# Kernel optimization log

Hardware: AMD Instinct MI355X
Metric: run time of the kernel (lower is better)

## Reference

```python
import jax, jax.numpy as jnp
import numpy as np

# TT configuration (matches init_kwargs)
P = (100, 100, 100)      # tt_p_shapes, prod = num_embeddings = 1e6
Q = (4, 4, 8)            # tt_q_shapes, prod = embedding_dim = 128
R = (1, 32, 32, 1)       # tt_ranks padded with boundary 1s
D = 128                  # embedding_dim
B = 4096                 # batch size (number of bags)
H = 50                   # pooling factor (history length)
NNZ = B * H              # total indices


def setup_inputs() -> dict:
    key = jax.random.key(0)
    k1, k2, k3, k4 = jax.random.split(key, 4)
    # TT cores, stored flattened along trailing dims like TT-Rec:
    # core_i : [p_i, r_i * q_i * r_{i+1}]
    sigma = 0.1
    core0 = sigma * jax.random.normal(k1, (P[0], R[0] * Q[0] * R[1]), dtype=jnp.float32)
    core1 = sigma * jax.random.normal(k2, (P[1], R[1] * Q[1] * R[2]), dtype=jnp.float32)
    core2 = sigma * jax.random.normal(k3, (P[2], R[2] * Q[2] * R[3]), dtype=jnp.float32)
    indices = jax.random.randint(k4, (NNZ,), 0, P[0] * P[1] * P[2], dtype=jnp.int32)
    lengths = jnp.full((B,), H, dtype=jnp.int32)
    return {"indices": indices, "lengths": lengths,
            "core0": core0, "core1": core1, "core2": core2}


def reference(indices, lengths, core0, core1, core2):
    n = indices.shape[0]
    # mixed-radix decomposition of flat row index over p-shapes
    i1 = indices // (P[1] * P[2])
    i2 = (indices // P[2]) % P[1]
    i3 = indices % P[2]
    # gather per-index TT core slices
    a = core0[i1].reshape(n, Q[0], R[1])          # [n, q1, r1]
    b = core1[i2].reshape(n, R[1], Q[1], R[2])    # [n, r1, q2, r2]
    c = core2[i3].reshape(n, R[2], Q[2])          # [n, r2, q3]
    # TT contraction chain reconstructing each embedding row
    ab = jnp.einsum('nar,nrbs->nabs', a, b).reshape(n, Q[0] * Q[1], R[2])  # [n, q1*q2, r2]
    emb = jnp.einsum('nms,nsc->nmc', ab, c).reshape(n, D)                  # [n, D]
    # bag sum-pooling: rowidx = repeat_interleave(arange(B), lengths)
    batch = lengths.shape[0]
    rowidx = jnp.repeat(jnp.arange(batch, dtype=jnp.int32), lengths,
                        total_repeat_length=n)
    out = jax.ops.segment_sum(emb, rowidx, num_segments=batch)             # [B, D]
    return out
```

## Files before the change

### kernel.cpp

```cpp
#include <hip/hip_runtime.h>
#include <hip/hip_bf16.h>


#define P0 100
#define P1 100
#define P2 100
#define Q0 4
#define Q1 4
#define Q2 8
#define DIM 128
#define NPAIR (P0 * P1)

typedef __attribute__((ext_vector_type(8))) short short8v;
typedef __attribute__((ext_vector_type(4))) float f32x4;

__global__ __launch_bounds__(128) void prep(const int* __restrict__ lengths, int B,
                                            const float* __restrict__ core0,
                                            const float* __restrict__ core1,
                                            const float* __restrict__ core2,
                                            int* __restrict__ offsets,
                                            __hip_bfloat16* __restrict__ bfrag,
                                            __hip_bfloat16* __restrict__ ab) {
    int bid = blockIdx.x;
    int t = threadIdx.x;
    if (bid == 0) {
        __shared__ int part[128];
        int per = (B + 127) / 128;
        int s = 0;
        for (int k = 0; k < per; ++k) {
            int i = t * per + k;
            s += (i < B) ? lengths[i] : 0;
        }
        part[t] = s;
        __syncthreads();
        for (int d = 1; d < 128; d <<= 1) {
            int v = (t >= d) ? part[t - d] : 0;
            __syncthreads();
            part[t] += v;
            __syncthreads();
        }
        int run = part[t] - s;
        for (int k = 0; k < per; ++k) {
            int i = t * per + k;
            if (i < B) { offsets[i] = run; run += lengths[i]; }
        }
        if (t == 127) offsets[B] = part[127];
    } else if (bid <= P2) {
        if (t < 64 && !(t & 8)) {
            int i3 = bid - 1;
            int h = t >> 4, c3 = t & 7;
            const float* crow = core2 + (size_t)i3 * (32 * Q2);
            __hip_bfloat16* o = bfrag + (size_t)i3 * 256 + h * 64 + c3 * 8;
#pragma unroll
            for (int j = 0; j < 8; ++j)
                o[j] = __float2bfloat16(crow[(h * 8 + j) * Q2 + c3]);
        }
    } else {
        int p12 = bid - 1 - P2;
        int i1 = p12 / P1;
        int i2 = p12 - i1 * P1;
        __shared__ float a_lds[128];
        a_lds[t] = core0[i1 * 128 + t];
        __syncthreads();
        const float* brow = core1 + (size_t)i2 * 4096;
        float acc0 = 0.f, acc1 = 0.f, acc2 = 0.f, acc3 = 0.f;
#pragma unroll
        for (int r = 0; r < 32; ++r) {
            float bv = brow[r * 128 + t];
            acc0 += a_lds[r] * bv;
            acc1 += a_lds[32 + r] * bv;
            acc2 += a_lds[64 + r] * bv;
            acc3 += a_lds[96 + r] * bv;
        }
        __hip_bfloat16* o = ab + (size_t)p12 * 512;
        o[t]       = __float2bfloat16(acc0);
        o[128 + t] = __float2bfloat16(acc1);
        o[256 + t] = __float2bfloat16(acc2);
        o[384 + t] = __float2bfloat16(acc3);
    }
}

__global__ __launch_bounds__(256, 6) void bag_pool(const int* __restrict__ indices, int n,
                                                   const int* __restrict__ offsets, int B,
                                                   const char* __restrict__ ab,
                                                   const char* __restrict__ bfrag,
                                                   float* __restrict__ out) {
    int w = threadIdx.x >> 6;
    int lane = threadIdx.x & 63;
    int bag = blockIdx.x * 2 + (w >> 1);
    int half = w & 1;

    int start = 0, end = 0;
    if (bag < B) {
        start = offsets[bag];
        end = offsets[bag + 1];
        if (bag == B - 1 && end < n) end = n;
        if (end > n) end = n;
        if (start > n) start = n;
        if (end < start) end = start;
    }
    int cnt = end - start;
    int c0 = (cnt + 1) >> 1;
    int mystart = start + (half ? c0 : 0);
    int mycnt = half ? (cnt - c0) : c0;

    int aoff = (lane & 15) * 64 + (lane >> 4) * 16;
    int boff = (lane >> 4) * 128 + (lane & 7) * 16;

    f32x4 acc0 = {0.f, 0.f, 0.f, 0.f};
    f32x4 acc1 = {0.f, 0.f, 0.f, 0.f};
    f32x4 acc2 = {0.f, 0.f, 0.f, 0.f};
    f32x4 acc3 = {0.f, 0.f, 0.f, 0.f};

    for (int cb = 0; cb < mycnt; cb += 64) {
        int m = mycnt - cb;
        if (m > 64) m = 64;
        unsigned idx = 0;
        if (lane < m) idx = (unsigned)indices[mystart + cb + lane];
        unsigned p = idx / 100u;
        unsigned i3 = idx - p * 100u;
        int abo = (int)(p << 10);
        int bfo = (int)(i3 << 9);

        int j = 0;
        for (; j + 3 < m; j += 4) {
            int A0 = __shfl(abo, j),     B0 = __shfl(bfo, j);
            int A1 = __shfl(abo, j + 1), B1 = __shfl(bfo, j + 1);
            int A2 = __shfl(abo, j + 2), B2 = __shfl(bfo, j + 2);
            int A3 = __shfl(abo, j + 3), B3 = __shfl(bfo, j + 3);
            short8v a0 = *(const short8v*)(ab + A0 + aoff);
            short8v b0 = *(const short8v*)(bfrag + B0 + boff);
            short8v a1 = *(const short8v*)(ab + A1 + aoff);
            short8v b1 = *(const short8v*)(bfrag + B1 + boff);
            short8v a2 = *(const short8v*)(ab + A2 + aoff);
            short8v b2 = *(const short8v*)(bfrag + B2 + boff);
            short8v a3 = *(const short8v*)(ab + A3 + aoff);
            short8v b3 = *(const short8v*)(bfrag + B3 + boff);
            acc0 = __builtin_amdgcn_mfma_f32_16x16x32_bf16(a0, b0, acc0, 0, 0, 0);
            acc1 = __builtin_amdgcn_mfma_f32_16x16x32_bf16(a1, b1, acc1, 0, 0, 0);
            acc2 = __builtin_amdgcn_mfma_f32_16x16x32_bf16(a2, b2, acc2, 0, 0, 0);
            acc3 = __builtin_amdgcn_mfma_f32_16x16x32_bf16(a3, b3, acc3, 0, 0, 0);
        }
        for (; j < m; ++j) {
            int A0 = __shfl(abo, j), B0 = __shfl(bfo, j);
            short8v a0 = *(const short8v*)(ab + A0 + aoff);
            short8v b0 = *(const short8v*)(bfrag + B0 + boff);
            acc0 = __builtin_amdgcn_mfma_f32_16x16x32_bf16(a0, b0, acc0, 0, 0, 0);
        }
    }
    f32x4 acc = (acc0 + acc1) + (acc2 + acc3);

    __shared__ f32x4 red[2][64];
    if (half) red[w >> 1][lane] = acc;
    __syncthreads();
    if (!half) {
        acc += red[w >> 1][lane];
        int col = lane & 15;
        if (bag < B && col < 8) {
            int rb = (lane >> 4) * 4;
            float* orow = out + (size_t)bag * DIM;
#pragma unroll
            for (int q = 0; q < 4; ++q)
                orow[(rb + q) * 8 + col] = acc[q];
        }
    }
}

__global__ __launch_bounds__(128) void fallback_pool(const int* __restrict__ indices,
                                                     int n, int B,
                                                     const float* __restrict__ core0,
                                                     const float* __restrict__ core1,
                                                     const float* __restrict__ core2,
                                                     float* __restrict__ out) {
    int bag = blockIdx.x;
    int d = threadIdx.x;
    int m = d >> 3, c3 = d & 7;
    int a_ = m >> 2, b_ = m & 3;
    int H = n / B;
    float acc = 0.f;
    for (int j = bag * H; j < (bag + 1) * H; ++j) {
        int idx = indices[j];
        int i1 = idx / (P1 * P2);
        int rem = idx - i1 * (P1 * P2);
        int i2 = rem / P2;
        int i3 = rem - i2 * P2;
        const float* a = core0 + (size_t)i1 * 128;
        const float* b = core1 + (size_t)i2 * 4096;
        const float* c = core2 + (size_t)i3 * 256;
        float e = 0.f;
        for (int s = 0; s < 32; ++s) {
            float abv = 0.f;
            for (int r = 0; r < 32; ++r)
                abv += a[a_ * 32 + r] * b[r * 128 + b_ * 32 + s];
            e += abv * c[s * 8 + c3];
        }
        acc += e;
    }
    out[(size_t)bag * DIM + d] = acc;
}

extern "C" void kernel_launch(void* const* d_in, const int* in_sizes, int n_in,
                              void* d_out, int out_size, void* d_ws, size_t ws_size,
                              hipStream_t stream) {
    const int* indices = (const int*)d_in[0];
    const int* lengths = (const int*)d_in[1];
    const float* core0 = (const float*)d_in[2];
    const float* core1 = (const float*)d_in[3];
    const float* core2 = (const float*)d_in[4];
    float* out = (float*)d_out;
    int n = in_sizes[0];
    int B = in_sizes[1];

    const size_t OFF_OFFSETS = 0;
    const size_t OFF_BFRAG = 32768;
    const size_t OFF_AB = 131072;
    const size_t REQ = OFF_AB + (size_t)NPAIR * 1024;

    if (ws_size >= REQ) {
        int* offsets = (int*)((char*)d_ws + OFF_OFFSETS);
        __hip_bfloat16* bfragp = (__hip_bfloat16*)((char*)d_ws + OFF_BFRAG);
        __hip_bfloat16* abt = (__hip_bfloat16*)((char*)d_ws + OFF_AB);

        prep<<<1 + P2 + NPAIR, 128, 0, stream>>>(lengths, B, core0, core1, core2,
                                                 offsets, bfragp, abt);
        bag_pool<<<(B + 1) / 2, 256, 0, stream>>>(indices, n, offsets, B,
                                                  (const char*)abt, (const char*)bfragp, out);
    } else {
        fallback_pool<<<B, 128, 0, stream>>>(indices, n, B, core0, core1, core2, out);
    }
}
```

Measured before the change: 44.17 us.

## Compute core0×core1 product table with MFMA in far fewer prep blocks

The precomputed ab table (core0 slice times core1 slice for every (i1,i2) pair) was built by 10000 small blocks doing scalar FMAs. It is now built by 200 blocks of 256 threads. Each wave holds a bf16 fragment of one core1 slice in registers and loops over all i1 values, issuing one bf16 MFMA per group of four i1 rows and scattering the results into the same ab layout. This cuts launch and scheduling overhead and core1 reloads. It adds bf16 rounding of the inputs before the product (previously fp32 accumulate then round) and uses strided 2-byte scattered stores.

```diff
diff --git a/kernel.cpp b/kernel.cpp
--- a/kernel.cpp
+++ b/kernel.cpp
@@ -14,7 +14,13 @@
 typedef __attribute__((ext_vector_type(8))) short short8v;
 typedef __attribute__((ext_vector_type(4))) float f32x4;
 
-__global__ __launch_bounds__(128) void prep(const int* __restrict__ lengths, int B,
+__device__ inline short f2bf(float x) {
+    union { __hip_bfloat16 h; short s; } u;
+    u.h = __float2bfloat16(x);
+    return u.s;
+}
+
+__global__ __launch_bounds__(256) void prep(const int* __restrict__ lengths, int B,
                                             const float* __restrict__ core0,
                                             const float* __restrict__ core1,
                                             const float* __restrict__ core2,
@@ -24,8 +30,8 @@
     int bid = blockIdx.x;
     int t = threadIdx.x;
     if (bid == 0) {
-        __shared__ int part[128];
-        int per = (B + 127) / 128;
+        __shared__ int part[256];
+        int per = (B + 255) / 256;
         int s = 0;
         for (int k = 0; k < per; ++k) {
             int i = t * per + k;
@@ -33,7 +39,7 @@
         }
         part[t] = s;
         __syncthreads();
-        for (int d = 1; d < 128; d <<= 1) {
+        for (int d = 1; d < 256; d <<= 1) {
             int v = (t >= d) ? part[t - d] : 0;
             __syncthreads();
             part[t] += v;
@@ -44,7 +50,7 @@
             int i = t * per + k;
             if (i < B) { offsets[i] = run; run += lengths[i]; }
         }
-        if (t == 127) offsets[B] = part[127];
+        if (t == 255) offsets[B] = part[255];
     } else if (bid <= P2) {
         if (t < 64 && !(t & 8)) {
             int i3 = bid - 1;
@@ -56,27 +62,36 @@
                 o[j] = __float2bfloat16(crow[(h * 8 + j) * Q2 + c3]);
         }
     } else {
-        int p12 = bid - 1 - P2;
-        int i1 = p12 / P1;
-        int i2 = p12 - i1 * P1;
-        __shared__ float a_lds[128];
-        a_lds[t] = core0[i1 * 128 + t];
-        __syncthreads();
-        const float* brow = core1 + (size_t)i2 * 4096;
-        float acc0 = 0.f, acc1 = 0.f, acc2 = 0.f, acc3 = 0.f;
-#pragma unroll
-        for (int r = 0; r < 32; ++r) {
-            float bv = brow[r * 128 + t];
-            acc0 += a_lds[r] * bv;
-            acc1 += a_lds[32 + r] * bv;
-            acc2 += a_lds[64 + r] * bv;
-            acc3 += a_lds[96 + r] * bv;
-        }
-        __hip_bfloat16* o = ab + (size_t)p12 * 512;
-        o[t]       = __float2bfloat16(acc0);
-        o[128 + t] = __float2bfloat16(acc1);
-        o[256 + t] = __float2bfloat16(acc2);
-        o[384 + t] = __float2bfloat16(acc3);
+        int g = bid - 1 - P2;
+        int i2 = g >> 1;
+        int w = t >> 6, lane = t & 63;
+        int ct = (g & 1) * 4 + w;
+        int h = lane >> 4;
+        int c16 = lane & 15;
+
+        const float* bbase = core1 + (size_t)i2 * 4096 + (h * 8) * 128 + ct * 16 + c16;
+        short8v bfr;
+#pragma unroll
+        for (int j = 0; j < 8; ++j) bfr[j] = f2bf(bbase[j * 128]);
+
+        int col = ct * 16 + c16;
+        for (int rt = 0; rt < 25; ++rt) {
+            const float* abase = core0 + (size_t)(rt * 4 + (c16 >> 2)) * 128
+                                 + (c16 & 3) * 32 + h * 8;
+            f32x4 x0 = *(const f32x4*)abase;
+            f32x4 x1 = *(const f32x4*)(abase + 4);
+            short8v afr;
+#pragma unroll
+            for (int j = 0; j < 4; ++j) { afr[j] = f2bf(x0[j]); afr[j + 4] = f2bf(x1[j]); }
+
+            f32x4 d = __builtin_amdgcn_mfma_f32_16x16x32_bf16(
+                afr, bfr, (f32x4){0.f, 0.f, 0.f, 0.f}, 0, 0, 0);
+
+            __hip_bfloat16* dst = ab + (size_t)((rt * 4 + h) * P1 + i2) * 512
+                                  + (col >> 5) * 32 + (col & 31);
+#pragma unroll
+            for (int q = 0; q < 4; ++q) dst[q * 128] = __float2bfloat16(d[q]);
+        }
     }
 }
 
@@ -221,8 +236,8 @@
         __hip_bfloat16* bfragp = (__hip_bfloat16*)((char*)d_ws + OFF_BFRAG);
         __hip_bfloat16* abt = (__hip_bfloat16*)((char*)d_ws + OFF_AB);
 
-        prep<<<1 + P2 + NPAIR, 128, 0, stream>>>(lengths, B, core0, core1, core2,
-                                                 offsets, bfragp, abt);
+        prep<<<1 + P2 + 200, 256, 0, stream>>>(lengths, B, core0, core1, core2,
+                                               offsets, bfragp, abt);
         bag_pool<<<(B + 1) / 2, 256, 0, stream>>>(indices, n, offsets, B,
                                                   (const char*)abt, (const char*)bfragp, out);
     } else {
```

Result: faster. 43.29 us, median of 2 (-2.0%).
